# Kernel optimization log

Measured on AMD Instinct MI355X. Metric: run time of the kernel, lower is better.

The kernel has to match this reference:

```python
import jax, jax.numpy as jnp
import numpy as np

B, T, C, H = 8, 4096, 1024, 128  # batch, seq, n_embd, head_size


def setup_inputs() -> dict:
    key = jax.random.key(0)
    ks = jax.random.split(key, 4)
    std = 1.0 / np.sqrt(C)
    return {
        "x": jax.random.normal(ks[0], (B, T, C), dtype=jnp.float32),
        "Wq": jax.random.normal(ks[1], (C, H), dtype=jnp.float32) * std,
        "bq": jnp.zeros((H,), dtype=jnp.float32),
        "Wk": jax.random.normal(ks[2], (C, H), dtype=jnp.float32) * std,
        "bk": jnp.zeros((H,), dtype=jnp.float32),
        "Wv": jax.random.normal(ks[3], (C, H), dtype=jnp.float32) * std,
        "bv": jnp.zeros((H,), dtype=jnp.float32),
    }


def reference(x, Wq, bq, Wk, bk, Wv, bv):
    # Q, K, V projections: [B, T, H]
    q = x @ Wq + bq
    k = x @ Wk + bk
    v = x @ Wv + bv
    scale = jnp.asarray(H, x.dtype) ** -0.5
    # scaled attention scores: [B, T, T]
    wei = jnp.einsum("bqh,bkh->bqk", q, k) * scale
    # causal mask: position q attends to k <= q
    causal = jnp.tril(jnp.ones((T, T), dtype=bool))
    wei = jnp.where(causal[None, :, :], wei, jnp.finfo(x.dtype).min)
    wei = jax.nn.softmax(wei, axis=-1)
    # dropout p=0.0 (eval) -> identity
    out = jnp.einsum("bqk,bkh->bqh", wei, v)  # [B, T, H]
    return out
```

## Files before the change

### kernel.cpp

```cpp
#include <hip/hip_runtime.h>
#include <hip/hip_bf16.h>

typedef __attribute__((ext_vector_type(8))) short short8;
typedef __attribute__((ext_vector_type(4))) float floatx4;
typedef __attribute__((ext_vector_type(4))) unsigned int uintx4;

#define BB 8
#define TT 4096
#define CC 1024
#define HH 128
#define BT (BB * TT)

__device__ __forceinline__ unsigned short f2bf(float f) {
    unsigned int u = __float_as_uint(f);
    u += 0x7fffu + ((u >> 16) & 1u);
    return (unsigned short)(u >> 16);
}

__global__ void conv_w(const float* __restrict__ Wq, const float* __restrict__ Wk,
                       const float* __restrict__ Wv, unsigned short* __restrict__ Wt) {
    __shared__ float tile[32][33];
    const int w = blockIdx.z, nt = blockIdx.y, kt = blockIdx.x;
    const int tx = threadIdx.x, ty = threadIdx.y;
    const float* W = (w == 0) ? Wq : ((w == 1) ? Wk : Wv);
#pragma unroll
    for (int i = 0; i < 4; ++i)
        tile[ty + 8 * i][tx] = W[(kt * 32 + ty + 8 * i) * HH + nt * 32 + tx];
    __syncthreads();
#pragma unroll
    for (int i = 0; i < 4; ++i)
        Wt[w * (HH * CC) + (nt * 32 + ty + 8 * i) * CC + kt * 32 + tx] = f2bf(tile[tx][ty + 8 * i]);
}

__global__ __launch_bounds__(256) void proj_gemm(
    const float* __restrict__ x, const unsigned short* __restrict__ Wt,
    const float* __restrict__ bq, const float* __restrict__ bk, const float* __restrict__ bv,
    unsigned short* __restrict__ Qb, unsigned short* __restrict__ Kb,
    unsigned short* __restrict__ Vt) {
    __shared__ unsigned short As[64 * 72];
    __shared__ unsigned short Bs[384 * 72];
    const int mbase = blockIdx.x * 64;
    const int tid = threadIdx.x, lane = tid & 63, wv = tid >> 6;
    const int quad = lane >> 4, l15 = lane & 15;
    const int arow = tid >> 2, aseg = tid & 3;

    floatx4 acc[24];
#pragma unroll
    for (int i = 0; i < 24; ++i) {
        floatx4 z = {0.f, 0.f, 0.f, 0.f};
        acc[i] = z;
    }

    for (int kt = 0; kt < 16; ++kt) {
        {
            const float* xp = x + (long)(mbase + arow) * CC + kt * 64 + aseg * 16;
            floatx4 f0 = *(const floatx4*)(xp);
            floatx4 f1 = *(const floatx4*)(xp + 4);
            floatx4 f2 = *(const floatx4*)(xp + 8);
            floatx4 f3 = *(const floatx4*)(xp + 12);
            uintx4 p0, p1;
            p0[0] = (unsigned)f2bf(f0[0]) | ((unsigned)f2bf(f0[1]) << 16);
            p0[1] = (unsigned)f2bf(f0[2]) | ((unsigned)f2bf(f0[3]) << 16);
            p0[2] = (unsigned)f2bf(f1[0]) | ((unsigned)f2bf(f1[1]) << 16);
            p0[3] = (unsigned)f2bf(f1[2]) | ((unsigned)f2bf(f1[3]) << 16);
            p1[0] = (unsigned)f2bf(f2[0]) | ((unsigned)f2bf(f2[1]) << 16);
            p1[1] = (unsigned)f2bf(f2[2]) | ((unsigned)f2bf(f2[3]) << 16);
            p1[2] = (unsigned)f2bf(f3[0]) | ((unsigned)f2bf(f3[1]) << 16);
            p1[3] = (unsigned)f2bf(f3[2]) | ((unsigned)f2bf(f3[3]) << 16);
            *(uintx4*)&As[arow * 72 + aseg * 16] = p0;
            *(uintx4*)&As[arow * 72 + aseg * 16 + 8] = p1;
        }
#pragma unroll
        for (int h = 0; h < 12; ++h) {
            int c = tid + h * 256;
            int row = c >> 3, seg = c & 7;
            *(uintx4*)&Bs[row * 72 + seg * 8] =
                *(const uintx4*)(Wt + (long)row * CC + kt * 64 + seg * 8);
        }
        __syncthreads();
        short8 af0 = *(const short8*)&As[(wv * 16 + l15) * 72 + quad * 8];
        short8 af1 = *(const short8*)&As[(wv * 16 + l15) * 72 + 32 + quad * 8];
#pragma unroll
        for (int ni = 0; ni < 24; ++ni) {
            short8 b0 = *(const short8*)&Bs[(ni * 16 + l15) * 72 + quad * 8];
            short8 b1 = *(const short8*)&Bs[(ni * 16 + l15) * 72 + 32 + quad * 8];
            acc[ni] = __builtin_amdgcn_mfma_f32_16x16x32_bf16(af0, b0, acc[ni], 0, 0, 0);
            acc[ni] = __builtin_amdgcn_mfma_f32_16x16x32_bf16(af1, b1, acc[ni], 0, 0, 0);
        }
        __syncthreads();
    }

#pragma unroll
    for (int ni = 0; ni < 24; ++ni) {
        int col = ni * 16 + l15;
        int wsel = col >> 7, h = col & 127;
        float bval = (wsel == 0) ? bq[h] : ((wsel == 1) ? bk[h] : bv[h]);
#pragma unroll
        for (int r = 0; r < 4; ++r) {
            int row = mbase + wv * 16 + quad * 4 + r;
            float v = acc[ni][r] + bval;
            if (wsel == 0) {
                Qb[(long)row * HH + h] = f2bf(v * 0.08838834764831845f);
            } else if (wsel == 1) {
                Kb[(long)row * HH + h] = f2bf(v);
            } else {
                int bb = row >> 12, t = row & 4095;
                Vt[(long)bb * (HH * TT) + (long)h * TT + t] = f2bf(v);
            }
        }
    }
}

__global__ __launch_bounds__(256) void attn(
    const unsigned short* __restrict__ Qb, const unsigned short* __restrict__ Kb,
    const unsigned short* __restrict__ Vt, unsigned short* __restrict__ Op0,
    unsigned short* __restrict__ Op1, float2* __restrict__ Ml) {
    __shared__ unsigned short Ks[64 * 136];
    __shared__ unsigned short Vs[128 * 72];
    __shared__ unsigned short Ps[4 * 16 * 72];
    const int gid = blockIdx.x;
    const int qb = 63 - (gid >> 4);
    const int sub = gid & 15;
    const int b = sub & 7;
    const int s = sub >> 3;
    const int mid = (qb + 1) >> 1;
    const int lo = (s == 0) ? 0 : mid;
    const int hi = (s == 0) ? mid : qb + 1;
    const int tid = threadIdx.x, lane = tid & 63, wv = tid >> 6;
    const int quad = lane >> 4, l15 = lane & 15;

    short8 qf[4];
    {
        const unsigned short* qp = Qb + ((long)b * TT + qb * 64 + wv * 16 + l15) * HH + quad * 8;
#pragma unroll
        for (int ks = 0; ks < 4; ++ks) qf[ks] = *(const short8*)(qp + ks * 32);
    }
    floatx4 o[8];
#pragma unroll
    for (int i = 0; i < 8; ++i) {
        floatx4 z = {0.f, 0.f, 0.f, 0.f};
        o[i] = z;
    }
    float m_r[4] = {-1e30f, -1e30f, -1e30f, -1e30f};
    float l_r[4] = {0.f, 0.f, 0.f, 0.f};

    const unsigned short* Kbb = Kb + (long)b * TT * HH;
    const unsigned short* Vbb = Vt + (long)b * HH * TT;
    unsigned short* Pw = &Ps[wv * 16 * 72];

    for (int kb = lo; kb < hi; ++kb) {
#pragma unroll
        for (int h = 0; h < 4; ++h) {
            int c = tid + h * 256;
            int kr = c >> 4, kc = c & 15;
            *(uintx4*)&Ks[kr * 136 + kc * 8] =
                *(const uintx4*)(Kbb + (long)(kb * 64 + kr) * HH + kc * 8);
            int vr = c >> 3, vc = c & 7;
            *(uintx4*)&Vs[vr * 72 + vc * 8] =
                *(const uintx4*)(Vbb + (long)vr * TT + kb * 64 + vc * 8);
        }
        __syncthreads();

        floatx4 sArr[4];
#pragma unroll
        for (int nt = 0; nt < 4; ++nt) {
            floatx4 z = {0.f, 0.f, 0.f, 0.f};
            sArr[nt] = z;
        }
#pragma unroll
        for (int ks = 0; ks < 4; ++ks)
#pragma unroll
            for (int nt = 0; nt < 4; ++nt) {
                short8 kf = *(const short8*)&Ks[(nt * 16 + l15) * 136 + ks * 32 + quad * 8];
                sArr[nt] = __builtin_amdgcn_mfma_f32_16x16x32_bf16(qf[ks], kf, sArr[nt], 0, 0, 0);
            }

        if (kb == qb) {
            int rowl = wv * 16 + quad * 4;
#pragma unroll
            for (int nt = 0; nt < 4; ++nt) {
                int col = nt * 16 + l15;
#pragma unroll
                for (int r = 0; r < 4; ++r)
                    if (col > rowl + r) sArr[nt][r] = -1e30f;
            }
        }

        float alpha[4];
#pragma unroll
        for (int r = 0; r < 4; ++r) {
            float mx = fmaxf(fmaxf(sArr[0][r], sArr[1][r]), fmaxf(sArr[2][r], sArr[3][r]));
#pragma unroll
            for (int off = 1; off < 16; off <<= 1) mx = fmaxf(mx, __shfl_xor(mx, off));
            float mnew = fmaxf(m_r[r], mx);
            alpha[r] = __expf(m_r[r] - mnew);
            m_r[r] = mnew;
            float rs = 0.f;
#pragma unroll
            for (int nt = 0; nt < 4; ++nt) {
                float p = __expf(sArr[nt][r] - mnew);
                sArr[nt][r] = p;
                rs += p;
            }
#pragma unroll
            for (int off = 1; off < 16; off <<= 1) rs += __shfl_xor(rs, off);
            l_r[r] = l_r[r] * alpha[r] + rs;
        }
#pragma unroll
        for (int hn = 0; hn < 8; ++hn)
#pragma unroll
            for (int r = 0; r < 4; ++r) o[hn][r] *= alpha[r];

#pragma unroll
        for (int nt = 0; nt < 4; ++nt)
#pragma unroll
            for (int r = 0; r < 4; ++r)
                Pw[(quad * 4 + r) * 72 + nt * 16 + l15] = f2bf(sArr[nt][r]);

#pragma unroll
        for (int k2 = 0; k2 < 2; ++k2) {
            short8 pf = *(const short8*)&Pw[l15 * 72 + k2 * 32 + quad * 8];
#pragma unroll
            for (int hn = 0; hn < 8; ++hn) {
                short8 vf = *(const short8*)&Vs[(hn * 16 + l15) * 72 + k2 * 32 + quad * 8];
                o[hn] = __builtin_amdgcn_mfma_f32_16x16x32_bf16(pf, vf, o[hn], 0, 0, 0);
            }
        }
        __syncthreads();
    }

    unsigned short* Op = (s == 0) ? Op0 : Op1;
    long rbase = (long)b * TT + qb * 64 + wv * 16 + quad * 4;
    if (hi > lo) {
#pragma unroll
        for (int hn = 0; hn < 8; ++hn)
#pragma unroll
            for (int r = 0; r < 4; ++r)
                Op[(rbase + r) * HH + hn * 16 + l15] = f2bf(o[hn][r] / l_r[r]);
    }
    if (l15 == 0) {
#pragma unroll
        for (int r = 0; r < 4; ++r) {
            float2 ml;
            ml.x = m_r[r];
            ml.y = l_r[r];
            Ml[(long)s * BT + rbase + r] = ml;
        }
    }
}

__global__ __launch_bounds__(256) void merge_kern(
    const unsigned short* __restrict__ Op0, const unsigned short* __restrict__ Op1,
    const float2* __restrict__ Ml, float* __restrict__ out) {
    long e = ((long)blockIdx.x * 256 + threadIdx.x) * 8;
    long row = e >> 7;
    float2 a = Ml[row];
    float2 c = Ml[BT + row];
    float ms = fmaxf(a.x, c.x);
    float w0 = a.y * __expf(a.x - ms);
    float w1 = c.y * __expf(c.x - ms);
    float inv = 1.f / (w0 + w1);
    w0 *= inv;
    w1 *= inv;
    uintx4 p0 = *(const uintx4*)(Op0 + e);
    uintx4 p1 = *(const uintx4*)(Op1 + e);
    floatx4 o0, o1;
#pragma unroll
    for (int j = 0; j < 4; ++j) {
        float a0 = __uint_as_float(p0[j] << 16);
        float a1 = __uint_as_float(p0[j] & 0xffff0000u);
        float b0 = __uint_as_float(p1[j] << 16);
        float b1 = __uint_as_float(p1[j] & 0xffff0000u);
        if (j < 2) {
            o0[2 * j] = w0 * a0 + w1 * b0;
            o0[2 * j + 1] = w0 * a1 + w1 * b1;
        } else {
            o1[2 * (j - 2)] = w0 * a0 + w1 * b0;
            o1[2 * (j - 2) + 1] = w0 * a1 + w1 * b1;
        }
    }
    *(floatx4*)(out + e) = o0;
    *(floatx4*)(out + e + 4) = o1;
}

extern "C" void kernel_launch(void* const* d_in, const int* in_sizes, int n_in,
                              void* d_out, int out_size, void* d_ws, size_t ws_size,
                              hipStream_t stream) {
    const float* x  = (const float*)d_in[0];
    const float* Wq = (const float*)d_in[1];
    const float* bq = (const float*)d_in[2];
    const float* Wk = (const float*)d_in[3];
    const float* bk = (const float*)d_in[4];
    const float* Wv = (const float*)d_in[5];
    const float* bv = (const float*)d_in[6];
    float* out = (float*)d_out;

    char* ws = (char*)d_ws;
    unsigned short* Wt  = (unsigned short*)(ws);
    unsigned short* Qb  = (unsigned short*)(ws + 1048576);
    unsigned short* Kb  = (unsigned short*)(ws + 9437184);
    unsigned short* Vt  = (unsigned short*)(ws + 17825792);
    unsigned short* Op0 = (unsigned short*)(ws + 26214400);
    unsigned short* Op1 = (unsigned short*)(ws + 34603008);
    float2*         Ml  = (float2*)(ws + 42991616);

    conv_w<<<dim3(32, 4, 3), dim3(32, 8), 0, stream>>>(Wq, Wk, Wv, Wt);
    proj_gemm<<<512, 256, 0, stream>>>(x, Wt, bq, bk, bv, Qb, Kb, Vt);
    attn<<<1024, 256, 0, stream>>>(Qb, Kb, Vt, Op0, Op1, Ml);
    merge_kern<<<2048, 256, 0, stream>>>(Op0, Op1, Ml, out);
}
```

Baseline: 337.6 us.

## Use async global-to-LDS loads with XOR swizzle, retile projection GEMM, exp2 softmax

The K/V tiles in attention and the weight tiles in the projection GEMM are now loaded with global_load_lds straight into unpadded, XOR-swizzled shared memory instead of passing through registers. The projection GEMM is retiled so each wave computes 4x6 MFMA tiles and reuses A fragments across N. The V output is transposed through LDS so it can be stored as wide vectors instead of scattered 2-byte writes. Softmax folds log2(e) into the Q scale and uses exp2f, and the P staging buffer shrinks. The swizzle and lane-to-address mapping for the async loads must match exactly, or results will be wrong.

```diff
diff --git a/kernel.cpp b/kernel.cpp
--- a/kernel.cpp
+++ b/kernel.cpp
@@ -2,6 +2,7 @@
 #include <hip/hip_bf16.h>
 
 typedef __attribute__((ext_vector_type(8))) short short8;
+typedef __attribute__((ext_vector_type(4))) short shortx4;
 typedef __attribute__((ext_vector_type(4))) float floatx4;
 typedef __attribute__((ext_vector_type(4))) unsigned int uintx4;
 
@@ -15,6 +16,12 @@
     unsigned int u = __float_as_uint(f);
     u += 0x7fffu + ((u >> 16) & 1u);
     return (unsigned short)(u >> 16);
+}
+
+__device__ __forceinline__ void async16(const unsigned short* g, unsigned short* l) {
+    __builtin_amdgcn_global_load_lds(
+        (const __attribute__((address_space(1))) unsigned int*)g,
+        (__attribute__((address_space(3))) unsigned int*)l, 16, 0, 0);
 }
 
 __global__ void conv_w(const float* __restrict__ Wq, const float* __restrict__ Wk,
@@ -38,18 +45,22 @@
     unsigned short* __restrict__ Qb, unsigned short* __restrict__ Kb,
     unsigned short* __restrict__ Vt) {
     __shared__ unsigned short As[64 * 72];
-    __shared__ unsigned short Bs[384 * 72];
+    __shared__ unsigned short Bs[384 * 64];
     const int mbase = blockIdx.x * 64;
     const int tid = threadIdx.x, lane = tid & 63, wv = tid >> 6;
     const int quad = lane >> 4, l15 = lane & 15;
     const int arow = tid >> 2, aseg = tid & 3;
-
-    floatx4 acc[24];
-#pragma unroll
-    for (int i = 0; i < 24; ++i) {
-        floatx4 z = {0.f, 0.f, 0.f, 0.f};
-        acc[i] = z;
-    }
+    const int brow = lane >> 3;
+    const int wc = (lane & 7) ^ (brow & 7);
+
+    floatx4 acc[4][6];
+#pragma unroll
+    for (int i = 0; i < 4; ++i)
+#pragma unroll
+        for (int j = 0; j < 6; ++j) {
+            floatx4 z = {0.f, 0.f, 0.f, 0.f};
+            acc[i][j] = z;
+        }
 
     for (int kt = 0; kt < 16; ++kt) {
         {
@@ -72,41 +83,64 @@
         }
 #pragma unroll
         for (int h = 0; h < 12; ++h) {
-            int c = tid + h * 256;
-            int row = c >> 3, seg = c & 7;
-            *(uintx4*)&Bs[row * 72 + seg * 8] =
-                *(const uintx4*)(Wt + (long)row * CC + kt * 64 + seg * 8);
+            int grp = 4 * h + wv;
+            async16(Wt + (long)(grp * 8 + brow) * CC + kt * 64 + wc * 8, &Bs[grp * 512]);
         }
         __syncthreads();
-        short8 af0 = *(const short8*)&As[(wv * 16 + l15) * 72 + quad * 8];
-        short8 af1 = *(const short8*)&As[(wv * 16 + l15) * 72 + 32 + quad * 8];
-#pragma unroll
-        for (int ni = 0; ni < 24; ++ni) {
-            short8 b0 = *(const short8*)&Bs[(ni * 16 + l15) * 72 + quad * 8];
-            short8 b1 = *(const short8*)&Bs[(ni * 16 + l15) * 72 + 32 + quad * 8];
-            acc[ni] = __builtin_amdgcn_mfma_f32_16x16x32_bf16(af0, b0, acc[ni], 0, 0, 0);
-            acc[ni] = __builtin_amdgcn_mfma_f32_16x16x32_bf16(af1, b1, acc[ni], 0, 0, 0);
+#pragma unroll
+        for (int ks = 0; ks < 2; ++ks) {
+            short8 af[4];
+#pragma unroll
+            for (int mi = 0; mi < 4; ++mi)
+                af[mi] = *(const short8*)&As[(mi * 16 + l15) * 72 + ks * 32 + quad * 8];
+#pragma unroll
+            for (int ni = 0; ni < 6; ++ni) {
+                short8 bfr = *(const short8*)&Bs[(wv * 96 + ni * 16 + l15) * 64 +
+                                                 (((ks * 4 + quad) ^ (l15 & 7)) * 8)];
+#pragma unroll
+                for (int mi = 0; mi < 4; ++mi)
+                    acc[mi][ni] = __builtin_amdgcn_mfma_f32_16x16x32_bf16(af[mi], bfr, acc[mi][ni], 0, 0, 0);
+            }
         }
         __syncthreads();
     }
 
-#pragma unroll
-    for (int ni = 0; ni < 24; ++ni) {
-        int col = ni * 16 + l15;
-        int wsel = col >> 7, h = col & 127;
-        float bval = (wsel == 0) ? bq[h] : ((wsel == 1) ? bk[h] : bv[h]);
-#pragma unroll
-        for (int r = 0; r < 4; ++r) {
-            int row = mbase + wv * 16 + quad * 4 + r;
-            float v = acc[ni][r] + bval;
-            if (wsel == 0) {
-                Qb[(long)row * HH + h] = f2bf(v * 0.08838834764831845f);
-            } else if (wsel == 1) {
-                Kb[(long)row * HH + h] = f2bf(v);
-            } else {
-                int bb = row >> 12, t = row & 4095;
-                Vt[(long)bb * (HH * TT) + (long)h * TT + t] = f2bf(v);
-            }
+    const float qscale = 0.08838834764831845f * 1.4426950408889634f;
+    unsigned short* Tw = &As[wv * 1152];
+#pragma unroll
+    for (int ni = 0; ni < 6; ++ni) {
+        int f = wv * 6 + ni;
+        int col = f * 16 + l15;
+        int h = col & 127;
+        if (f < 16) {
+            float bval = (f < 8) ? bq[h] : bk[h];
+            unsigned short* dst = (f < 8) ? Qb : Kb;
+#pragma unroll
+            for (int mi = 0; mi < 4; ++mi)
+#pragma unroll
+                for (int r = 0; r < 4; ++r) {
+                    int row = mbase + mi * 16 + quad * 4 + r;
+                    float v = acc[mi][ni][r] + bval;
+                    if (f < 8) v *= qscale;
+                    dst[(long)row * HH + h] = f2bf(v);
+                }
+        } else {
+            float bval = bv[h];
+#pragma unroll
+            for (int mi = 0; mi < 4; ++mi) {
+                shortx4 pk;
+#pragma unroll
+                for (int r = 0; r < 4; ++r) pk[r] = (short)f2bf(acc[mi][ni][r] + bval);
+                *(shortx4*)&Tw[l15 * 72 + mi * 16 + quad * 4] = pk;
+            }
+            int th = lane >> 2, seg = lane & 3;
+            uintx4 q0 = *(const uintx4*)&Tw[th * 72 + seg * 16];
+            uintx4 q1 = *(const uintx4*)&Tw[th * 72 + seg * 16 + 8];
+            int hg = (f - 16) * 16 + th;
+            int bb = mbase >> 12, t0 = (mbase & 4095) + seg * 16;
+            unsigned short* vp = Vt + (long)bb * (HH * TT) + (long)hg * TT + t0;
+            *(uintx4*)(vp) = q0;
+            *(uintx4*)(vp + 8) = q1;
         }
     }
 }
@@ -115,9 +149,9 @@
     const unsigned short* __restrict__ Qb, const unsigned short* __restrict__ Kb,
     const unsigned short* __restrict__ Vt, unsigned short* __restrict__ Op0,
     unsigned short* __restrict__ Op1, float2* __restrict__ Ml) {
-    __shared__ unsigned short Ks[64 * 136];
-    __shared__ unsigned short Vs[128 * 72];
-    __shared__ unsigned short Ps[4 * 16 * 72];
+    __shared__ unsigned short Ks[64 * 128];
+    __shared__ unsigned short Vs[128 * 64];
+    __shared__ unsigned short Ps[4 * 16 * 40];
     const int gid = blockIdx.x;
     const int qb = 63 - (gid >> 4);
     const int sub = gid & 15;
@@ -144,21 +178,22 @@
     float m_r[4] = {-1e30f, -1e30f, -1e30f, -1e30f};
     float l_r[4] = {0.f, 0.f, 0.f, 0.f};
 
-    const unsigned short* Kbb = Kb + (long)b * TT * HH;
-    const unsigned short* Vbb = Vt + (long)b * HH * TT;
-    unsigned short* Pw = &Ps[wv * 16 * 72];
+    const int kc = l15 ^ (4 * wv + quad);
+    const unsigned short* Kg = Kb + (long)b * TT * HH + ((long)lo * 64 + 4 * wv + quad) * HH + kc * 8;
+    const int vrow = lane >> 3;
+    const int vc = (lane & 7) ^ (vrow & 7);
+    const unsigned short* Vg = Vt + (long)b * HH * TT + (long)(8 * wv + vrow) * TT + lo * 64 + vc * 8;
+    unsigned short* Pw = &Ps[wv * 640];
 
     for (int kb = lo; kb < hi; ++kb) {
 #pragma unroll
         for (int h = 0; h < 4; ++h) {
-            int c = tid + h * 256;
-            int kr = c >> 4, kc = c & 15;
-            *(uintx4*)&Ks[kr * 136 + kc * 8] =
-                *(const uintx4*)(Kbb + (long)(kb * 64 + kr) * HH + kc * 8);
-            int vr = c >> 3, vc = c & 7;
-            *(uintx4*)&Vs[vr * 72 + vc * 8] =
-                *(const uintx4*)(Vbb + (long)vr * TT + kb * 64 + vc * 8);
-        }
+            int grp = 4 * h + wv;
+            async16(Kg + (long)h * (16 * HH), &Ks[grp * 512]);
+            async16(Vg + (long)h * 32 * TT, &Vs[grp * 512]);
+        }
+        Kg += (long)64 * HH;
+        Vg += 64;
         __syncthreads();
 
         floatx4 sArr[4];
@@ -171,7 +206,7 @@
         for (int ks = 0; ks < 4; ++ks)
 #pragma unroll
             for (int nt = 0; nt < 4; ++nt) {
-                short8 kf = *(const short8*)&Ks[(nt * 16 + l15) * 136 + ks * 32 + quad * 8];
+                short8 kf = *(const short8*)&Ks[(nt * 16 + l15) * 128 + (((ks * 4 + quad) ^ l15) * 8)];
                 sArr[nt] = __builtin_amdgcn_mfma_f32_16x16x32_bf16(qf[ks], kf, sArr[nt], 0, 0, 0);
             }
 
@@ -193,12 +228,12 @@
 #pragma unroll
             for (int off = 1; off < 16; off <<= 1) mx = fmaxf(mx, __shfl_xor(mx, off));
             float mnew = fmaxf(m_r[r], mx);
-            alpha[r] = __expf(m_r[r] - mnew);
+            alpha[r] = exp2f(m_r[r] - mnew);
             m_r[r] = mnew;
             float rs = 0.f;
 #pragma unroll
             for (int nt = 0; nt < 4; ++nt) {
-                float p = __expf(sArr[nt][r] - mnew);
+                float p = exp2f(sArr[nt][r] - mnew);
                 sArr[nt][r] = p;
                 rs += p;
             }
@@ -212,17 +247,17 @@
             for (int r = 0; r < 4; ++r) o[hn][r] *= alpha[r];
 
 #pragma unroll
-        for (int nt = 0; nt < 4; ++nt)
-#pragma unroll
-            for (int r = 0; r < 4; ++r)
-                Pw[(quad * 4 + r) * 72 + nt * 16 + l15] = f2bf(sArr[nt][r]);
-
-#pragma unroll
         for (int k2 = 0; k2 < 2; ++k2) {
-            short8 pf = *(const short8*)&Pw[l15 * 72 + k2 * 32 + quad * 8];
+#pragma unroll
+            for (int ntl = 0; ntl < 2; ++ntl)
+#pragma unroll
+                for (int r = 0; r < 4; ++r)
+                    Pw[(quad * 4 + r) * 40 + ntl * 16 + l15] = f2bf(sArr[k2 * 2 + ntl][r]);
+            short8 pf = *(const short8*)&Pw[l15 * 40 + quad * 8];
 #pragma unroll
             for (int hn = 0; hn < 8; ++hn) {
-                short8 vf = *(const short8*)&Vs[(hn * 16 + l15) * 72 + k2 * 32 + quad * 8];
+                short8 vf = *(const short8*)&Vs[(hn * 16 + l15) * 64 +
+                                                (((k2 * 4 + quad) ^ (l15 & 7)) * 8)];
                 o[hn] = __builtin_amdgcn_mfma_f32_16x16x32_bf16(pf, vf, o[hn], 0, 0, 0);
             }
         }
@@ -257,8 +292,8 @@
     float2 a = Ml[row];
     float2 c = Ml[BT + row];
     float ms = fmaxf(a.x, c.x);
-    float w0 = a.y * __expf(a.x - ms);
-    float w1 = c.y * __expf(c.x - ms);
+    float w0 = a.y * exp2f(a.x - ms);
+    float w1 = c.y * exp2f(c.x - ms);
     float inv = 1.f / (w0 + w1);
     w0 *= inv;
     w1 *= inv;
```

Result: slower. 355.3 us (+5.3%).
